# Kernel tuning notes

Measured on AMD Instinct MI355X. Metric: run time of the kernel, lower is better.

## Reference

```python
import jax, jax.numpy as jnp
import numpy as np
from jax import lax

B, S, DM = 2, 2048, 2048
H, HKV, D = 16, 4, 128          # heads, kv heads, head_dim = DM // H
CLAMP_MAX = 0.95


def setup_inputs() -> dict:
    key = jax.random.key(0)
    k0, k1, k2, k3 = jax.random.split(key, 4)
    w_scale = 2 ** (-2.5) * (6.0 / (DM + DM)) ** 0.5  # xavier_uniform gain 2^-2.5 scale
    return {
        "hidden_states": jax.random.normal(k0, (B, S, DM), dtype=jnp.float32),
        "Wq": jax.random.uniform(k1, (DM, DM), jnp.float32, -w_scale, w_scale),
        "bq": jnp.zeros((DM,), jnp.float32),
        "Wk": jax.random.uniform(k2, (HKV * D, DM), jnp.float32, -w_scale, w_scale),
        "bk": jnp.zeros((HKV * D,), jnp.float32),
        "Wv": jax.random.uniform(k3, (HKV * D, DM), jnp.float32, -w_scale, w_scale),
        "bv": jnp.zeros((HKV * D,), jnp.float32),
    }


def _gla_forward(hidden_states, Wq, bq, Wk, bk, Wv, bv):
    b, s, _ = hidden_states.shape
    q = hidden_states @ Wq.T + bq                      # [b, s, H*D]
    k = hidden_states @ Wk.T + bk                      # [b, s, HKV*D]
    v = hidden_states @ Wv.T + bv                      # [b, s, HKV*D]
    q = q.reshape(b, s, H, D).transpose(0, 2, 1, 3)    # [b, H, s, D]
    k = k.reshape(b, s, HKV, D).transpose(0, 2, 1, 3)  # [b, HKV, s, D]
    v = v.reshape(b, s, HKV, D).transpose(0, 2, 1, 3)
    rep = H // HKV                                     # repeat_kv (GQA)
    k = jnp.repeat(k, rep, axis=1)                     # [b, H, s, D]
    v = jnp.repeat(v, rep, axis=1)
    q = jax.nn.relu(q)                                 # q_feature_map
    # layer_idx == 0 gate path: k = clamp(sigmoid(k), max=0.95); g = log(1 - k)
    kf = jnp.minimum(jax.nn.sigmoid(k.astype(jnp.float32)), CLAMP_MAX)
    g = jnp.log1p(-kf)                                 # log-space decay, g <= log(0.05) < 0 ... 0
    k = kf.astype(v.dtype)
    scale = D ** -0.5                                  # fla gla default scale = head_dim**-0.5
    q = (q * scale).astype(v.dtype)

    # GLA recurrence over time: S_t = exp(g_t)[:,None] * S_{t-1} + k_t^T v_t ; o_t = q_t S_t
    qs = q.transpose(2, 0, 1, 3)   # [s, b, H, D]
    ks = k.transpose(2, 0, 1, 3)
    vs = v.transpose(2, 0, 1, 3)
    gs = g.transpose(2, 0, 1, 3)

    def step(state, inp):           # state: [b, H, D, D] (key_dim x value_dim)
        qt, kt, vt, gt = inp
        state = state * jnp.exp(gt)[..., :, None] + kt[..., :, None] * vt[..., None, :]
        ot = jnp.einsum('bhd,bhde->bhe', qt, state)
        return state, ot

    S0 = jnp.zeros((b, H, D, D), jnp.float32)
    _, o = lax.scan(step, S0, (qs, ks, vs, gs))        # o: [s, b, H, D]
    o = o.transpose(1, 0, 2, 3).reshape(b, s, H * D)   # 'b h l d -> b l (h d)'
    return o


def reference(hidden_states, Wq, bq, Wk, bk, Wv, bv):
    return _gla_forward(hidden_states, Wq, bq, Wk, bk, Wv, bv)
```

## Files before the change

kernel.cpp:

```cpp
#include <hip/hip_runtime.h>
#include <math.h>

#define B_ 2
#define S_ 2048
#define DM_ 2048
#define H_ 16
#define HKV_ 4
#define D_ 128
#define NKV_ 512
#define M_ 4096
#define CHK_ 32
#define NC_ 64
#define SCALE_ 0.08838834764831845f
#define CLAMP_ 0.95f

typedef unsigned short u16;
typedef u16 ushortx8 __attribute__((ext_vector_type(8)));
typedef __bf16 bf16x8 __attribute__((ext_vector_type(8)));
typedef float f32x4 __attribute__((ext_vector_type(4)));

#define ASYNC16(gsrc, ldst) \
  __builtin_amdgcn_global_load_lds((const __attribute__((address_space(1))) void*)(gsrc), \
                                   (__attribute__((address_space(3))) void*)(ldst), 16, 0, 0)
#define SBAR()    __builtin_amdgcn_s_barrier()
#define WAITV(n)  asm volatile("s_waitcnt vmcnt(" #n ")" ::: "memory")

__device__ __forceinline__ u16 f2b(float x){
  unsigned u = __float_as_uint(x);
  return (u16)((u + 0x7FFFu + ((u >> 16) & 1u)) >> 16);
}
__device__ __forceinline__ float b2f(u16 h){
  return __uint_as_float(((unsigned)h) << 16);
}
__device__ __forceinline__ bf16x8 ld8(const u16* p){
  return __builtin_bit_cast(bf16x8, *(const ushortx8*)p);
}
__device__ __forceinline__ f32x4 mfma16(bf16x8 a, bf16x8 b, f32x4 c){
  return __builtin_amdgcn_mfma_f32_16x16x32_bf16(a, b, c, 0, 0, 0);
}

__global__ void k_cvt_all(const float* __restrict__ hs, const float* __restrict__ Wq,
                          const float* __restrict__ Wk, const float* __restrict__ Wv,
                          u16* __restrict__ hsb, u16* __restrict__ wcb){
  int i = blockIdx.x * blockDim.x + threadIdx.x;
  const float* src; u16* dst;
  if (i < 1048576)      { src = hs + (size_t)i * 8;               dst = hsb + (size_t)i * 8; }
  else if (i < 1572864) { int j = i - 1048576; src = Wq + (size_t)j * 8; dst = wcb + (size_t)j * 8; }
  else if (i < 1703936) { int j = i - 1572864; src = Wk + (size_t)j * 8; dst = wcb + 4194304 + (size_t)j * 8; }
  else                  { int j = i - 1703936; src = Wv + (size_t)j * 8; dst = wcb + 5242880 + (size_t)j * 8; }
  const float4* p = (const float4*)src;
  float4 a = p[0], c = p[1];
  ushortx8 o;
  o[0]=f2b(a.x); o[1]=f2b(a.y); o[2]=f2b(a.z); o[3]=f2b(a.w);
  o[4]=f2b(c.x); o[5]=f2b(c.y); o[6]=f2b(c.z); o[7]=f2b(c.w);
  *(ushortx8*)dst = o;
}

__launch_bounds__(256, 2)
__global__ void k_gemm(const u16* __restrict__ A, const u16* __restrict__ W,
                       const float* __restrict__ bq, const float* __restrict__ bk,
                       const float* __restrict__ bv,
                       u16* __restrict__ qp, u16* __restrict__ kp,
                       float* __restrict__ gG, u16* __restrict__ vT){
  __shared__ u16 L[3 * 8192];
  const int tid = threadIdx.x;
  const int wid = tid >> 6, lane = tid & 63;
  const int m0 = blockIdx.y * 128, n0 = blockIdx.x * 128;
  const int wr = (wid >> 1) * 64, wc = (wid & 1) * 64;
  const int lr = lane & 15;

  int offA[4], offB[4];
  #pragma unroll
  for (int m = 0; m < 4; ++m)
    offA[m] = (wr + m * 16 + lr) * 32 + (((lane >> 4) ^ (lr & 3)) << 3);
  #pragma unroll
  for (int n = 0; n < 4; ++n)
    offB[n] = (wc + n * 16 + lr) * 32 + (((lane >> 4) ^ (lr & 3)) << 3);

  const int srow = wid * 32 + (lane >> 2);
  const int scol = (((lane & 3) ^ ((lane >> 2) & 3)) << 3);
  const u16* gA = A + (size_t)(m0 + srow) * DM_ + scol;
  const u16* gW = W + (size_t)(n0 + srow) * DM_ + scol;
  const int fo = wid * 1024;

#define STG(db, kk0) \
  ASYNC16(gA + (kk0),             L + (db) + fo); \
  ASYNC16(gA + 16 * DM_ + (kk0),  L + (db) + fo + 512); \
  ASYNC16(gW + (kk0),             L + (db) + 4096 + fo); \
  ASYNC16(gW + 16 * DM_ + (kk0),  L + (db) + 4096 + fo + 512)

  f32x4 acc[4][4] = {};

  STG(0, 0);
  STG(8192, 32);

  int sl_cur = 0, sl_st = 16384;
  for (int kt = 0; kt < 64; ++kt){
    WAITV(4);
    SBAR();
    const int k2 = ((kt + 2 < 64) ? kt + 2 : 63) * 32;
    STG(sl_st, k2);
    bf16x8 af[4], bfv[4];
    #pragma unroll
    for (int m = 0; m < 4; ++m) af[m]  = ld8(L + sl_cur + offA[m]);
    #pragma unroll
    for (int n = 0; n < 4; ++n) bfv[n] = ld8(L + sl_cur + 4096 + offB[n]);
    #pragma unroll
    for (int m = 0; m < 4; ++m)
      #pragma unroll
      for (int n = 0; n < 4; ++n)
        acc[m][n] = mfma16(af[m], bfv[n], acc[m][n]);
    sl_cur = (sl_cur == 16384) ? 0 : sl_cur + 8192;
    sl_st  = (sl_st  == 16384) ? 0 : sl_st  + 8192;
  }
#undef STG

  const int lg4 = lane >> 4;
  const int tn = blockIdx.x;
  if (tn < 16){
    #pragma unroll
    for (int i = 0; i < 4; ++i){
      const int rb = m0 + wr + i*16 + lg4*4;
      #pragma unroll
      for (int j = 0; j < 4; ++j){
        const int col = n0 + wc + j*16 + lr;
        const float bb = bq[col];
        #pragma unroll
        for (int r = 0; r < 4; ++r){
          float q = fmaxf(acc[i][j][r] + bb, 0.f) * SCALE_;
          qp[(size_t)(rb + r) * DM_ + col] = f2b(q);
        }
      }
    }
  } else if (tn < 20){
    #pragma unroll
    for (int i = 0; i < 4; ++i){
      const int rb = m0 + wr + i*16 + lg4*4;
      #pragma unroll
      for (int j = 0; j < 4; ++j){
        const int cc = n0 - DM_ + wc + j*16 + lr;
        const float bb = bk[cc];
        #pragma unroll
        for (int r = 0; r < 4; ++r){
          float x = acc[i][j][r] + bb;
          float kf = fminf(1.f / (1.f + __expf(-x)), CLAMP_);
          kp[(size_t)(rb + r) * NKV_ + cc] = f2b(kf);
          gG[(size_t)(rb + r) * NKV_ + cc] = log1pf(-kf);
        }
      }
    }
  } else {
    #pragma unroll
    for (int i = 0; i < 4; ++i){
      const int rb = m0 + wr + i*16 + lg4*4;
      const int bb_ = rb >> 11;
      const int srw = rb & 2047;
      #pragma unroll
      for (int j = 0; j < 4; ++j){
        const int cc = n0 - DM_ - NKV_ + wc + j*16 + lr;
        const float bias = bv[cc];
        const int kv = cc >> 7, e = cc & 127;
        ushort4 pk;
        pk.x = f2b(acc[i][j][0] + bias);
        pk.y = f2b(acc[i][j][1] + bias);
        pk.z = f2b(acc[i][j][2] + bias);
        pk.w = f2b(acc[i][j][3] + bias);
        *(ushort4*)(vT + (((size_t)(bb_ * HKV_ + kv) * D_ + e) * S_ + srw)) = pk;
      }
    }
  }
}

__global__ void k_cumsum(float* __restrict__ g, float* __restrict__ dec){
  const int c = blockIdx.x, b = blockIdx.z;
  const int col = blockIdx.y * 256 + threadIdx.x;
  const size_t base = ((size_t)b * S_ + (size_t)c * CHK_) * NKV_ + col;
  float v[CHK_];
  #pragma unroll
  for (int t = 0; t < CHK_; ++t) v[t] = g[base + (size_t)t * NKV_];
  float acc = 0.f;
  #pragma unroll
  for (int t = 0; t < CHK_; ++t){ acc += v[t]; v[t] = acc; }
  #pragma unroll
  for (int t = 0; t < CHK_; ++t) g[base + (size_t)t * NKV_] = v[t];
  const int kv = col >> 7, d = col & 127;
  dec[(((size_t)b * HKV_ + kv) * NC_ + c) * D_ + d] = __expf(acc);
}

__launch_bounds__(256, 2)
__global__ void k_dstate(const u16* __restrict__ kp, const float* __restrict__ G,
                         const u16* __restrict__ vT, u16* __restrict__ SSt){
  __shared__ float kex[CHK_][D_];
  __shared__ float vl[D_][CHK_ + 1];
  const int c = blockIdx.x, kv = blockIdx.y, b = blockIdx.z;
  const int tid = threadIdx.x;
  const int s0 = c * CHK_;
  const size_t gbase = ((size_t)b * S_ + s0) * NKV_ + kv * D_;
  for (int idx = tid; idx < CHK_ * D_; idx += 256){
    const int t = idx >> 7, d = idx & 127;
    const float Gt  = G[gbase + (size_t)t  * NKV_ + d];
    const float G31 = G[gbase + (size_t)31 * NKV_ + d];
    const float kf = b2f(kp[gbase + (size_t)t * NKV_ + d]);
    kex[t][d] = kf * __expf(G31 - Gt);
  }
  const size_t vbase = ((size_t)(b * HKV_ + kv) * D_) * S_ + s0;
  for (int idx = tid; idx < 512; idx += 256){
    const int e = idx >> 2, t8 = (idx & 3) * 8;
    ushortx8 vv = *(const ushortx8*)(vT + vbase + (size_t)e * S_ + t8);
    #pragma unroll
    for (int u = 0; u < 8; ++u) vl[e][t8 + u] = b2f(vv[u]);
  }
  __syncthreads();
  const int w = tid >> 6, lane = tid & 63;
  const int e = (w & 1) * 64 + lane;
  const int d0 = (w >> 1) * 64;
  float acc[64];
  #pragma unroll
  for (int i = 0; i < 64; ++i) acc[i] = 0.f;
  for (int t = 0; t < CHK_; ++t){
    const float vv = vl[e][t];
    const float4* kr = (const float4*)(&kex[t][d0]);
    #pragma unroll
    for (int i4 = 0; i4 < 16; ++i4){
      float4 kk = kr[i4];
      acc[i4*4+0] = fmaf(vv, kk.x, acc[i4*4+0]);
      acc[i4*4+1] = fmaf(vv, kk.y, acc[i4*4+1]);
      acc[i4*4+2] = fmaf(vv, kk.z, acc[i4*4+2]);
      acc[i4*4+3] = fmaf(vv, kk.w, acc[i4*4+3]);
    }
  }
  const size_t ob = (((size_t)(b * HKV_ + kv) * NC_ + c) * D_ + e) * D_ + d0;
  #pragma unroll
  for (int i8 = 0; i8 < 8; ++i8){
    ushortx8 o;
    #pragma unroll
    for (int u = 0; u < 8; ++u) o[u] = f2b(acc[i8*8 + u]);
    *(ushortx8*)(SSt + ob + i8*8) = o;
  }
}

__global__ void k_scan(u16* __restrict__ SSt, const float* __restrict__ dec){
  const int eg = blockIdx.x, kv = blockIdx.y, b = blockIdx.z;
  const int tid = threadIdx.x;
  const int e = eg * 4 + (tid >> 5);
  const int d4 = (tid & 31) * 4;
  const size_t base  = ((size_t)(b * HKV_ + kv) * NC_) * D_ * D_ + (size_t)e * D_ + d4;
  const size_t dbase = ((size_t)(b * HKV_ + kv) * NC_) * D_ + d4;
  float s0 = 0.f, s1 = 0.f, s2 = 0.f, s3 = 0.f;
  #pragma unroll 4
  for (int c = 0; c < NC_; ++c){
    const size_t off = base + (size_t)c * (D_ * D_);
    ushort4 dv = *(ushort4*)(SSt + off);
    float4 dc = *(const float4*)(dec + dbase + (size_t)c * D_);
    ushort4 wr;
    wr.x = f2b(s0); wr.y = f2b(s1); wr.z = f2b(s2); wr.w = f2b(s3);
    *(ushort4*)(SSt + off) = wr;
    s0 = s0 * dc.x + b2f(dv.x);
    s1 = s1 * dc.y + b2f(dv.y);
    s2 = s2 * dc.z + b2f(dv.z);
    s3 = s3 * dc.w + b2f(dv.w);
  }
}

#define L_SB   0
#define L_KE0  16384
#define L_KE1  18432
#define L_QEF  22528
#define L_QE1  38912
#define L_AM   47104
#define L_G15  51200
__global__ void __launch_bounds__(512)
k_out2(const u16* __restrict__ qp, const u16* __restrict__ kp,
       const float* __restrict__ G, const u16* __restrict__ vT,
       const u16* __restrict__ SSt, float* __restrict__ out){
  extern __shared__ u16 lds[];
  float* G15f = (float*)(lds + L_G15);
  const int c = blockIdx.x, kv = blockIdx.y, b = blockIdx.z;
  const int tid = threadIdx.x, wid = tid >> 6, lane = tid & 63;
  const int hh = wid >> 1, sub = wid & 1;
  const int s0 = c * CHK_;
  const int lr = lane & 15, lk = (lane >> 4) * 8;
  const size_t gb = ((size_t)b * S_ + s0) * NKV_ + kv * D_;
  const size_t qb0 = ((size_t)b * S_ + s0) * DM_ + (kv * 4) * D_;
  const size_t vb = ((size_t)(b * HKV_ + kv) * D_) * S_ + s0;

  {
    const u16* src = SSt + (((size_t)(b * HKV_ + kv) * NC_ + c) * (D_ * D_));
    #pragma unroll
    for (int is = 0; is < 4; ++is){
      const int fo = is * 4096 + wid * 512;
      ASYNC16(src + fo + lane * 8, lds + L_SB + fo);
    }
  }
  if (tid < 128) G15f[tid] = G[gb + (size_t)15 * NKV_ + tid];
  __syncthreads();

  for (int idx = tid; idx < 32 * 128; idx += 512){
    const int t = idx >> 7, d = idx & 127;
    const float Gt = G[gb + (size_t)t * NKV_ + d];
    const float kf = b2f(kp[gb + (size_t)t * NKV_ + d]);
    const float eGt = __expf(Gt);
    float qv[4];
    #pragma unroll
    for (int q4 = 0; q4 < 4; ++q4) qv[q4] = b2f(qp[qb0 + (size_t)t * DM_ + q4 * D_ + d]);
    #pragma unroll
    for (int q4 = 0; q4 < 4; ++q4) lds[L_QEF + q4 * 4096 + idx] = f2b(qv[q4] * eGt);
    if (t >= 16){
      const float r = __expf(Gt - G15f[d]);
      #pragma unroll
      for (int q4 = 0; q4 < 4; ++q4) lds[L_QE1 + q4 * 2048 + (t - 16) * 128 + d] = f2b(qv[q4] * r);
    }
    if (t < 16) lds[L_KE0 + idx] = f2b(kf * __expf(-Gt));
    lds[L_KE1 + idx] = f2b(kf * __expf(G15f[d] - Gt));
  }
  __syncthreads();

  const u16* QeF = lds + L_QEF + hh * 4096;
  const u16* Qe1 = lds + L_QE1 + hh * 2048;
  u16* Am = lds + L_AM + hh * 1024;
  if (sub == 0){
    f32x4 aU = {}, aL = {};
    #pragma unroll
    for (int kd = 0; kd < 4; ++kd){
      bf16x8 faU = ld8(&QeF[lr * 128 + kd * 32 + lk]);
      bf16x8 fbU = ld8(&lds[L_KE0 + lr * 128 + kd * 32 + lk]);
      aU = mfma16(faU, fbU, aU);
      bf16x8 faL = ld8(&Qe1[lr * 128 + kd * 32 + lk]);
      bf16x8 fbL = ld8(&lds[L_KE1 + (16 + lr) * 128 + kd * 32 + lk]);
      aL = mfma16(faL, fbL, aL);
    }
    #pragma unroll
    for (int r = 0; r < 4; ++r){
      const int rr = (lane >> 4) * 4 + r;
      float vU = aU[r]; if (lr > rr) vU = 0.f;
      Am[rr * 32 + lr] = f2b(vU);
      float vL = aL[r]; if (lr > rr) vL = 0.f;
      Am[(16 + rr) * 32 + 16 + lr] = f2b(vL);
    }
  } else {
    f32x4 aO = {};
    #pragma unroll
    for (int kd = 0; kd < 4; ++kd){
      bf16x8 fa = ld8(&Qe1[lr * 128 + kd * 32 + lk]);
      bf16x8 fb = ld8(&lds[L_KE1 + lr * 128 + kd * 32 + lk]);
      aO = mfma16(fa, fb, aO);
    }
    #pragma unroll
    for (int r = 0; r < 4; ++r){
      const int rr = (lane >> 4) * 4 + r;
      Am[(16 + rr) * 32 + lr] = f2b(aO[r]);
    }
    for (int i = lane; i < 256; i += 64) Am[(i >> 4) * 32 + 16 + (i & 15)] = 0;
  }
  __syncthreads();

  f32x4 o4[2][4] = {};
  const int ew = sub * 64;
  #pragma unroll
  for (int kd = 0; kd < 4; ++kd){
    bf16x8 fa0 = ld8(&QeF[(0  + lr) * 128 + kd * 32 + lk]);
    bf16x8 fa1 = ld8(&QeF[(16 + lr) * 128 + kd * 32 + lk]);
    #pragma unroll
    for (int j2 = 0; j2 < 4; ++j2){
      bf16x8 fb = ld8(&lds[L_SB + (ew + j2 * 16 + lr) * 128 + kd * 32 + lk]);
      o4[0][j2] = mfma16(fa0, fb, o4[0][j2]);
      o4[1][j2] = mfma16(fa1, fb, o4[1][j2]);
    }
  }
  {
    bf16x8 fa0 = ld8(&Am[lr * 32 + lk]);
    bf16x8 fa1 = ld8(&Am[(16 + lr) * 32 + lk]);
    #pragma unroll
    for (int j2 = 0; j2 < 4; ++j2){
      const u16* vr = vT + vb + (size_t)(ew + j2 * 16 + lr) * S_;
      bf16x8 fb = ld8(vr + lk);
      o4[0][j2] = mfma16(fa0, fb, o4[0][j2]);
      o4[1][j2] = mfma16(fa1, fb, o4[1][j2]);
    }
  }
  const int hD = (kv * 4 + hh) * D_;
  #pragma unroll
  for (int i2 = 0; i2 < 2; ++i2)
    #pragma unroll
    for (int j2 = 0; j2 < 4; ++j2)
      #pragma unroll
      for (int r = 0; r < 4; ++r){
        const int t = i2 * 16 + (lane >> 4) * 4 + r;
        const int e = ew + j2 * 16 + lr;
        out[((size_t)b * S_ + s0 + t) * DM_ + hD + e] = o4[i2][j2][r];
      }
}

extern "C" void kernel_launch(void* const* d_in, const int* in_sizes, int n_in,
                              void* d_out, int out_size, void* d_ws, size_t ws_size,
                              hipStream_t stream){
  const float* hs = (const float*)d_in[0];
  const float* Wq = (const float*)d_in[1];
  const float* bq = (const float*)d_in[2];
  const float* Wk = (const float*)d_in[3];
  const float* bk = (const float*)d_in[4];
  const float* Wv = (const float*)d_in[5];
  const float* bv = (const float*)d_in[6];
  char* ws = (char*)d_ws;
  u16*   hsb = (u16*)(ws);
  u16*   wcb = (u16*)(ws + 16777216);
  u16*   qp  = (u16*)(ws + 29360128);
  u16*   kp  = (u16*)(ws + 46137344);
  float* gG  = (float*)(ws + 50331648);
  u16*   vT  = (u16*)(ws + 58720256);
  float* dec = (float*)(ws + 62914560);
  u16*   SSt = (u16*)(ws + 63176704);
  float* out = (float*)d_out;

  hipFuncSetAttribute((const void*)k_out2,
                      hipFuncAttributeMaxDynamicSharedMemorySize, 102912);

  k_cvt_all<<<dim3(7168), 256, 0, stream>>>(hs, Wq, Wk, Wv, hsb, wcb);
  k_gemm<<<dim3(24, 32), 256, 0, stream>>>(hsb, wcb, bq, bk, bv, qp, kp, gG, vT);
  k_cumsum<<<dim3(NC_, 2, B_), 256, 0, stream>>>(gG, dec);
  k_dstate<<<dim3(NC_, HKV_, B_), 256, 0, stream>>>(kp, gG, vT, SSt);
  k_scan<<<dim3(32, HKV_, B_), 128, 0, stream>>>(SSt, dec);
  k_out2<<<dim3(NC_, HKV_, B_), 512, 102912, stream>>>(qp, kp, gG, vT, SSt, out);
}
```

Baseline: 151.6 us.

## Derive intra-chunk scaled Q/K tiles in registers and shrink k_out2 LDS footprint

```diff
diff --git a/kernel.cpp b/kernel.cpp
--- a/kernel.cpp
+++ b/kernel.cpp
@@ -37,6 +37,13 @@
 }
 __device__ __forceinline__ f32x4 mfma16(bf16x8 a, bf16x8 b, f32x4 c){
   return __builtin_amdgcn_mfma_f32_16x16x32_bf16(a, b, c, 0, 0, 0);
+}
+__device__ __forceinline__ bf16x8 scale8(bf16x8 v, const float* s){
+  ushortx8 u = __builtin_bit_cast(ushortx8, v);
+  ushortx8 o;
+  #pragma unroll
+  for (int j = 0; j < 8; ++j) o[j] = f2b(b2f(u[j]) * s[j]);
+  return __builtin_bit_cast(bf16x8, o);
 }
 
 __global__ void k_cvt_all(const float* __restrict__ hs, const float* __restrict__ Wq,
@@ -263,18 +270,16 @@
 }
 
 #define L_SB   0
-#define L_KE0  16384
-#define L_KE1  18432
-#define L_QEF  22528
-#define L_QE1  38912
-#define L_AM   47104
-#define L_G15  51200
+#define L_QEF  16384
+#define L_KE1  32768
+#define L_SF   36864
+#define LDS_OUT2_BYTES ((36864 + 256) * 2)
 __global__ void __launch_bounds__(512)
 k_out2(const u16* __restrict__ qp, const u16* __restrict__ kp,
        const float* __restrict__ G, const u16* __restrict__ vT,
        const u16* __restrict__ SSt, float* __restrict__ out){
   extern __shared__ u16 lds[];
-  float* G15f = (float*)(lds + L_G15);
+  float* sFf = (float*)(lds + L_SF);
   const int c = blockIdx.x, kv = blockIdx.y, b = blockIdx.z;
   const int tid = threadIdx.x, wid = tid >> 6, lane = tid & 63;
   const int hh = wid >> 1, sub = wid & 1;
@@ -292,43 +297,55 @@
       ASYNC16(src + fo + lane * 8, lds + L_SB + fo);
     }
   }
-  if (tid < 128) G15f[tid] = G[gb + (size_t)15 * NKV_ + tid];
-  __syncthreads();
+  const int dmy = tid & 127;
+  const float G15v = G[gb + (size_t)15 * NKV_ + dmy];
+  if (tid < 128) sFf[tid] = __expf(-G15v);
 
   for (int idx = tid; idx < 32 * 128; idx += 512){
-    const int t = idx >> 7, d = idx & 127;
-    const float Gt = G[gb + (size_t)t * NKV_ + d];
-    const float kf = b2f(kp[gb + (size_t)t * NKV_ + d]);
+    const int t = idx >> 7;
+    const float Gt = G[gb + (size_t)t * NKV_ + dmy];
+    const float kf = b2f(kp[gb + (size_t)t * NKV_ + dmy]);
     const float eGt = __expf(Gt);
     float qv[4];
     #pragma unroll
-    for (int q4 = 0; q4 < 4; ++q4) qv[q4] = b2f(qp[qb0 + (size_t)t * DM_ + q4 * D_ + d]);
+    for (int q4 = 0; q4 < 4; ++q4) qv[q4] = b2f(qp[qb0 + (size_t)t * DM_ + q4 * D_ + dmy]);
     #pragma unroll
     for (int q4 = 0; q4 < 4; ++q4) lds[L_QEF + q4 * 4096 + idx] = f2b(qv[q4] * eGt);
-    if (t >= 16){
-      const float r = __expf(Gt - G15f[d]);
-      #pragma unroll
-      for (int q4 = 0; q4 < 4; ++q4) lds[L_QE1 + q4 * 2048 + (t - 16) * 128 + d] = f2b(qv[q4] * r);
-    }
-    if (t < 16) lds[L_KE0 + idx] = f2b(kf * __expf(-Gt));
-    lds[L_KE1 + idx] = f2b(kf * __expf(G15f[d] - Gt));
+    lds[L_KE1 + idx] = f2b(kf * __expf(G15v - Gt));
   }
   __syncthreads();
 
+  float sreg[4][8];
+  #pragma unroll
+  for (int kd = 0; kd < 4; ++kd)
+    #pragma unroll
+    for (int j = 0; j < 8; ++j) sreg[kd][j] = sFf[kd * 32 + lk + j];
+
   const u16* QeF = lds + L_QEF + hh * 4096;
-  const u16* Qe1 = lds + L_QE1 + hh * 2048;
-  u16* Am = lds + L_AM + hh * 1024;
+  const u16* KE1 = lds + L_KE1;
+  f32x4 aU = {}, aL = {}, aO = {};
   if (sub == 0){
-    f32x4 aU = {}, aL = {};
     #pragma unroll
     for (int kd = 0; kd < 4; ++kd){
       bf16x8 faU = ld8(&QeF[lr * 128 + kd * 32 + lk]);
-      bf16x8 fbU = ld8(&lds[L_KE0 + lr * 128 + kd * 32 + lk]);
+      bf16x8 fbU = scale8(ld8(&KE1[lr * 128 + kd * 32 + lk]), sreg[kd]);
       aU = mfma16(faU, fbU, aU);
-      bf16x8 faL = ld8(&Qe1[lr * 128 + kd * 32 + lk]);
-      bf16x8 fbL = ld8(&lds[L_KE1 + (16 + lr) * 128 + kd * 32 + lk]);
+      bf16x8 faL = scale8(ld8(&QeF[(16 + lr) * 128 + kd * 32 + lk]), sreg[kd]);
+      bf16x8 fbL = ld8(&KE1[(16 + lr) * 128 + kd * 32 + lk]);
       aL = mfma16(faL, fbL, aL);
     }
+  } else {
+    #pragma unroll
+    for (int kd = 0; kd < 4; ++kd){
+      bf16x8 fa = scale8(ld8(&QeF[(16 + lr) * 128 + kd * 32 + lk]), sreg[kd]);
+      bf16x8 fb = ld8(&KE1[lr * 128 + kd * 32 + lk]);
+      aO = mfma16(fa, fb, aO);
+    }
+  }
+  __syncthreads();
+
+  u16* Am = lds + L_KE1 + hh * 1024;
+  if (sub == 0){
     #pragma unroll
     for (int r = 0; r < 4; ++r){
       const int rr = (lane >> 4) * 4 + r;
@@ -338,13 +355,6 @@
       Am[(16 + rr) * 32 + 16 + lr] = f2b(vL);
     }
   } else {
-    f32x4 aO = {};
-    #pragma unroll
-    for (int kd = 0; kd < 4; ++kd){
-      bf16x8 fa = ld8(&Qe1[lr * 128 + kd * 32 + lk]);
-      bf16x8 fb = ld8(&lds[L_KE1 + lr * 128 + kd * 32 + lk]);
-      aO = mfma16(fa, fb, aO);
-    }
     #pragma unroll
     for (int r = 0; r < 4; ++r){
       const int rr = (lane >> 4) * 4 + r;
@@ -413,12 +423,12 @@
   float* out = (float*)d_out;
 
   hipFuncSetAttribute((const void*)k_out2,
-                      hipFuncAttributeMaxDynamicSharedMemorySize, 102912);
+                      hipFuncAttributeMaxDynamicSharedMemorySize, LDS_OUT2_BYTES);
 
   k_cvt_all<<<dim3(7168), 256, 0, stream>>>(hs, Wq, Wk, Wv, hsb, wcb);
   k_gemm<<<dim3(24, 32), 256, 0, stream>>>(hsb, wcb, bq, bk, bv, qp, kp, gG, vT);
   k_cumsum<<<dim3(NC_, 2, B_), 256, 0, stream>>>(gG, dec);
   k_dstate<<<dim3(NC_, HKV_, B_), 256, 0, stream>>>(kp, gG, vT, SSt);
   k_scan<<<dim3(32, HKV_, B_), 128, 0, stream>>>(SSt, dec);
-  k_out2<<<dim3(NC_, HKV_, B_), 512, 102912, stream>>>(qp, kp, gG, vT, SSt, out);
-}
+  k_out2<<<dim3(NC_, HKV_, B_), 512, LDS_OUT2_BYTES, stream>>>(qp, kp, gG, vT, SSt, out);
+}
```

Result: faster. 145.6 us (-4.0%).
